# Kernel optimization log

Hardware: AMD Instinct MI355X
Metric: run time of the kernel (lower is better)

Reference implementation:

```python
import jax, jax.numpy as jnp
import numpy as np

N = 100000      # nodes
E = 800000      # edges (avg degree 8)
D_IN = 256      # input feature dim
D_H = 256       # hidden dim (hard-coded in module)
D_OUT = 128     # h_feats


def setup_inputs() -> dict:
    key = jax.random.key(0)
    ks = jax.random.split(key, 8)
    feat = jax.random.normal(ks[0], (N, D_IN), jnp.float32)
    src = jax.random.randint(ks[1], (E,), 0, N, dtype=jnp.int32)
    dst = jax.random.randint(ks[2], (E,), 0, N, dtype=jnp.int32)
    def lin(k, din, dout):
        return jax.random.normal(k, (din, dout), jnp.float32) / np.float32(np.sqrt(din))
    return {
        'feat': feat, 'src': src, 'dst': dst,
        'w_self1': lin(ks[3], D_IN, D_H), 'w_neigh1': lin(ks[4], D_IN, D_H),
        'b1': jnp.zeros((D_H,), jnp.float32),
        'w_self2': lin(ks[5], D_H, D_OUT), 'w_neigh2': lin(ks[6], D_H, D_OUT),
        'b2': jnp.zeros((D_OUT,), jnp.float32),
    }


def _sage_mean(h, src, dst, w_self, w_neigh, b):
    # DGL SAGEConv 'mean': rst = h @ W_self + mean_{in-neighbors}(h) @ W_neigh + b
    ones = jnp.ones((src.shape[0],), h.dtype)
    deg = jax.ops.segment_sum(ones, dst, num_segments=N)          # in-degree per node
    msum = jax.ops.segment_sum(h[src], dst, num_segments=N)      # [N, d] gather-scatter
    mean = msum / jnp.maximum(deg, 1.0)[:, None]                  # zero-degree -> 0
    return h @ w_self + mean @ w_neigh + b


def reference(feat, src, dst, w_self1, w_neigh1, b1, w_self2, w_neigh2, b2):
    h = jax.nn.relu(_sage_mean(feat, src, dst, w_self1, w_neigh1, b1))
    h = jax.nn.relu(_sage_mean(h, src, dst, w_self2, w_neigh2, b2))
    # F.normalize(h, dim=1): x / max(||x||_2, eps)
    norm = jnp.linalg.norm(h, axis=1, keepdims=True)
    return h / jnp.maximum(norm, 1e-12)
```

## Files before the change

### kernel.cpp

```cpp
#include <hip/hip_runtime.h>

#define DIN 256
#define DH  256
#define DOUT 128

typedef __attribute__((ext_vector_type(8))) short bf16x8;
typedef __attribute__((ext_vector_type(4))) float f32x4;
typedef __attribute__((ext_vector_type(2))) float f32x2;
typedef __attribute__((ext_vector_type(4))) unsigned short ushort4v;
typedef __attribute__((ext_vector_type(8))) unsigned short ushort8v;
typedef __attribute__((ext_vector_type(4))) unsigned int uint4v;

static __device__ __forceinline__ unsigned short f2bf(float x) {
    unsigned u = __float_as_uint(x);
    u += 0x7fffu + ((u >> 16) & 1u);
    return (unsigned short)(u >> 16);
}
static __device__ __forceinline__ float bf2f(unsigned short h) {
    return __uint_as_float(((unsigned)h) << 16);
}

static __device__ __forceinline__ void gload16(const unsigned short* g, void* l) {
    __builtin_amdgcn_global_load_lds(
        (const __attribute__((address_space(1))) unsigned int*)g,
        (__attribute__((address_space(3))) unsigned int*)l,
        16, 0, 0);
}

static __device__ __forceinline__ void cvt_unit(const float* __restrict__ feat,
                                                unsigned short* __restrict__ featb,
                                                unsigned int* __restrict__ feat8,
                                                long long i, long long ncHalf) {
    long long i2 = i + ncHalf;
    f32x4 v0 = __builtin_nontemporal_load((const f32x4*)feat + i);
    f32x4 v1 = __builtin_nontemporal_load((const f32x4*)feat + i2);
    ushort4v o0, o1;
    o0[0] = f2bf(v0[0]); o0[1] = f2bf(v0[1]); o0[2] = f2bf(v0[2]); o0[3] = f2bf(v0[3]);
    o1[0] = f2bf(v1[0]); o1[1] = f2bf(v1[1]); o1[2] = f2bf(v1[2]); o1[3] = f2bf(v1[3]);
    *((ushort4v*)featb + i)  = o0;
    *((ushort4v*)featb + i2) = o1;
    int u0 = __builtin_amdgcn_cvt_pk_fp8_f32(v0[0], v0[1], 0, 0);
    u0     = __builtin_amdgcn_cvt_pk_fp8_f32(v0[2], v0[3], u0, 1);
    int u1 = __builtin_amdgcn_cvt_pk_fp8_f32(v1[0], v1[1], 0, 0);
    u1     = __builtin_amdgcn_cvt_pk_fp8_f32(v1[2], v1[3], u1, 1);
    feat8[i]  = (unsigned)u0;
    feat8[i2] = (unsigned)u1;
}

__global__ void countcvt_kernel(const int* __restrict__ dst, int* __restrict__ cnt, int E, int bCnt,
                                const float* __restrict__ feat, unsigned short* __restrict__ featb,
                                unsigned int* __restrict__ feat8, long long ncHalf, int nA) {
    int b = blockIdx.x;
    int t0 = (int)((long long)b * bCnt / nA);
    int t1 = (int)((long long)(b + 1) * bCnt / nA);
    if (t1 > t0) {
        int e = t0 * 256 + threadIdx.x;
        if (e < E) atomicAdd(&cnt[dst[e]], 1);
    } else {
        long long i = (long long)(b - t0) * 256 + threadIdx.x;
        if (i < ncHalf) cvt_unit(feat, featb, feat8, i, ncHalf);
    }
}

__global__ void fillcvt_kernel(const int* __restrict__ src, const int* __restrict__ dst,
                               int* __restrict__ cursor, int* __restrict__ csr, int E, int bFill,
                               const float* __restrict__ feat, unsigned short* __restrict__ featb,
                               unsigned int* __restrict__ feat8, long long ncHalf,
                               int cvtOff, int bCvtB,
                               const float* __restrict__ w_self1, const float* __restrict__ w_neigh1,
                               const float* __restrict__ w_self2, const float* __restrict__ w_neigh2,
                               unsigned short* __restrict__ ws1t, unsigned short* __restrict__ wn1t,
                               unsigned short* __restrict__ wcat, int nB) {
    int b = blockIdx.x;
    int t0 = (int)((long long)b * bFill / nB);
    int t1 = (int)((long long)(b + 1) * bFill / nB);
    if (t1 > t0) {
        int e = t0 * 256 + threadIdx.x;
        if (e < E) {
            int d = dst[e];
            int p = atomicAdd(&cursor[d], 1);
            csr[p] = src[e];
        }
    } else {
        int j = b - t0;
        if (j < bCvtB) {
            long long i = (long long)(cvtOff + j) * 256 + threadIdx.x;
            if (i < ncHalf) cvt_unit(feat, featb, feat8, i, ncHalf);
        } else {
            int idx = (j - bCvtB) * 256 + threadIdx.x;
            if (idx < 65536) {
                int nn = idx >> 8, k = idx & 255;
                ws1t[idx] = f2bf(w_self1[k * 256 + nn]);
            } else if (idx < 131072) {
                int jj = idx - 65536; int nn = jj >> 8, k = jj & 255;
                wn1t[jj] = f2bf(w_neigh1[k * 256 + nn]);
            } else if (idx < 163840) {
                int jj = idx - 131072; int nn = jj >> 8, k = jj & 255;
                wcat[jj] = f2bf(w_neigh2[k * 128 + nn]);
            } else if (idx < 196608) {
                int jj = idx - 163840; int nn = jj >> 8, k = jj & 255;
                wcat[32768 + jj] = f2bf(w_self2[k * 128 + nn]);
            }
        }
    }
}

__global__ void block_sums_kernel(const int* __restrict__ cnt, int* __restrict__ partial, int N) {
    __shared__ int sdata[256];
    int t = threadIdx.x;
    int base = blockIdx.x * 1024;
    int s = 0;
#pragma unroll
    for (int j = 0; j < 4; ++j) {
        int i = base + t * 4 + j;
        if (i < N) s += cnt[i];
    }
    sdata[t] = s; __syncthreads();
    for (int o = 128; o; o >>= 1) {
        if (t < o) sdata[t] += sdata[t + o];
        __syncthreads();
    }
    if (t == 0) partial[blockIdx.x] = sdata[0];
}

__global__ void scan_block_kernel(int* __restrict__ cnt, const int* __restrict__ partial,
                                  int* __restrict__ off, int N, int E, int nb) {
    __shared__ int sdata[256];
    __shared__ int pbase;
    int b = blockIdx.x, t = threadIdx.x;

    int pv = (t < nb) ? partial[t] : 0;
    sdata[t] = pv; __syncthreads();
    for (int o = 1; o < 256; o <<= 1) {
        int y = (t >= o) ? sdata[t - o] : 0;
        __syncthreads();
        sdata[t] += y;
        __syncthreads();
    }
    if (t == 0) pbase = (b == 0) ? 0 : sdata[b - 1];
    __syncthreads();
    int base0 = pbase;
    __syncthreads();

    int base = b * 1024;
    int vals[4]; int local = 0;
#pragma unroll
    for (int j = 0; j < 4; ++j) {
        int i = base + t * 4 + j;
        vals[j] = (i < N) ? cnt[i] : 0;
        local += vals[j];
    }
    sdata[t] = local; __syncthreads();
    for (int o = 1; o < 256; o <<= 1) {
        int y = (t >= o) ? sdata[t - o] : 0;
        __syncthreads();
        sdata[t] += y;
        __syncthreads();
    }
    int run = sdata[t] - local + base0;
#pragma unroll
    for (int j = 0; j < 4; ++j) {
        int i = base + t * 4 + j;
        if (i < N) { off[i] = run; cnt[i] = run; }
        run += vals[j];
    }
    if (b == 0 && t == 0) off[N] = E;
}

__global__ void gather_mean256_kernel(const unsigned int* __restrict__ feat8, const int* __restrict__ off,
                                      const int* __restrict__ csr, unsigned short* __restrict__ agg, int N) {
    int wid  = (int)((blockIdx.x * (long long)blockDim.x + threadIdx.x) >> 6);
    int lane = threadIdx.x & 63;
    if (wid >= N) return;
    int start = off[wid], end = off[wid + 1];
    const int g   = lane >> 4;
    const int cl  = lane & 15;
    float a[16] = {};
    int e = start;
    for (; e + 7 < end; e += 8) {
        int s0 = csr[e + g], s1 = csr[e + 4 + g];
        uint4v v0 = *(const uint4v*)(feat8 + (long long)s0 * 64 + cl * 4);
        uint4v v1 = *(const uint4v*)(feat8 + (long long)s1 * 64 + cl * 4);
#pragma unroll
        for (int d = 0; d < 4; ++d) {
            f32x2 p0 = __builtin_amdgcn_cvt_pk_f32_fp8((int)v0[d], false);
            f32x2 p1 = __builtin_amdgcn_cvt_pk_f32_fp8((int)v0[d], true);
            f32x2 q0 = __builtin_amdgcn_cvt_pk_f32_fp8((int)v1[d], false);
            f32x2 q1 = __builtin_amdgcn_cvt_pk_f32_fp8((int)v1[d], true);
            a[d * 4 + 0] += p0[0] + q0[0];
            a[d * 4 + 1] += p0[1] + q0[1];
            a[d * 4 + 2] += p1[0] + q1[0];
            a[d * 4 + 3] += p1[1] + q1[1];
        }
    }
    for (; e < end; e += 4) {
        int idx = e + g;
        if (idx < end) {
            int s = csr[idx];
            uint4v v = *(const uint4v*)(feat8 + (long long)s * 64 + cl * 4);
#pragma unroll
            for (int d = 0; d < 4; ++d) {
                f32x2 p0 = __builtin_amdgcn_cvt_pk_f32_fp8((int)v[d], false);
                f32x2 p1 = __builtin_amdgcn_cvt_pk_f32_fp8((int)v[d], true);
                a[d * 4 + 0] += p0[0];
                a[d * 4 + 1] += p0[1];
                a[d * 4 + 2] += p1[0];
                a[d * 4 + 3] += p1[1];
            }
        }
    }
#pragma unroll
    for (int j = 0; j < 16; ++j) {
        a[j] += __shfl_xor(a[j], 16);
        a[j] += __shfl_xor(a[j], 32);
    }
    if (g == 0) {
        float inv = 1.0f / (float)max(end - start, 1);
        ushort8v o0, o1;
#pragma unroll
        for (int j = 0; j < 8; ++j) { o0[j] = f2bf(a[j] * inv); o1[j] = f2bf(a[8 + j] * inv); }
        unsigned short* dstp = agg + (long long)wid * 256 + cl * 16;
        *(ushort8v*)dstp       = o0;
        *(ushort8v*)(dstp + 8) = o1;
    }
}

__global__ __launch_bounds__(512)
void gemm1_kernel(const unsigned short* __restrict__ A,  const unsigned short* __restrict__ WT,
                  const unsigned short* __restrict__ A2, const unsigned short* __restrict__ WT2,
                  const float* __restrict__ bias, unsigned short* __restrict__ C, int M)
{
    const int K = 256;
    __shared__ __align__(16) char lds[2][24576];

    const int tid = threadIdx.x;
    const int wid = tid >> 6, lane = tid & 63;
    const int l15 = lane & 15, lg = lane >> 4;
    const int wr = wid >> 2, wc = wid & 3;
    const int row0 = blockIdx.x * 128;

    long long asrc; int adst;
    {
        int c = tid, r = c >> 2, s = c & 3;
        int kc = s ^ ((r >> 1) & 3);
        asrc = (long long)min(row0 + r, M - 1) * K + kc * 8;
        adst = c * 16;
    }
    long long bsrc[2]; int bdst[2];
#pragma unroll
    for (int i = 0; i < 2; ++i) {
        int c = wid * 128 + i * 64 + lane, r = c >> 2, s = c & 3;
        int kc = s ^ ((r >> 1) & 3);
        bsrc[i] = (long long)r * K + kc * 8;
        bdst[i] = 8192 + c * 16;
    }

    const int slot = (lg ^ ((l15 >> 1) & 3)) * 16;
    int aoff[4], boff[4];
#pragma unroll
    for (int m = 0; m < 4; ++m) aoff[m] = (wr * 64 + m * 16 + l15) * 64 + slot;
#pragma unroll
    for (int n = 0; n < 4; ++n) boff[n] = 8192 + (wc * 64 + n * 16 + l15) * 64 + slot;

    f32x4 acc[4][4] = {};

    auto stage = [&](int buf, int t) {
        const unsigned short* Ap = (t >= 8) ? A2 : A;
        const unsigned short* Wp = (t >= 8) ? WT2 : WT;
        int k0 = (t & 7) * 32;
        gload16(Ap + asrc + k0, &lds[buf][adst]);
        gload16(Wp + bsrc[0] + k0, &lds[buf][bdst[0]]);
        gload16(Wp + bsrc[1] + k0, &lds[buf][bdst[1]]);
    };

    stage(0, 0);
    __syncthreads();

    for (int t = 0; t < 16; ++t) {
        const int cur = t & 1;
        if (t + 1 < 16) stage(cur ^ 1, t + 1);
        const char* L = lds[cur];
        bf16x8 af[4], bfr[4];
#pragma unroll
        for (int m = 0; m < 4; ++m) af[m]  = *(const bf16x8*)(L + aoff[m]);
#pragma unroll
        for (int n = 0; n < 4; ++n) bfr[n] = *(const bf16x8*)(L + boff[n]);
#pragma unroll
        for (int m = 0; m < 4; ++m)
#pragma unroll
            for (int n = 0; n < 4; ++n)
                acc[m][n] = __builtin_amdgcn_mfma_f32_16x16x32_bf16(af[m], bfr[n], acc[m][n], 0, 0, 0);
        __syncthreads();
    }

#pragma unroll
    for (int m = 0; m < 4; ++m) {
#pragma unroll
        for (int rr = 0; rr < 4; ++rr) {
            int grow = row0 + wr * 64 + m * 16 + lg * 4 + rr;
            if (grow >= M) continue;
#pragma unroll
            for (int n = 0; n < 4; ++n) {
                int gcol = wc * 64 + n * 16 + l15;
                float v = fmaxf(acc[m][n][rr] + bias[gcol], 0.f);
                C[(long long)grow * 256 + gcol] = f2bf(v);
            }
        }
    }
}

__global__ __launch_bounds__(512)
void gemm23_kernel(const unsigned short* __restrict__ A, const unsigned short* __restrict__ WT,
                   const float* __restrict__ b2,
                   unsigned short* __restrict__ p2, unsigned short* __restrict__ self2, int M)
{
    const int K = 256;
    __shared__ __align__(16) char lds[2][24576];

    const int tid = threadIdx.x;
    const int wid = tid >> 6, lane = tid & 63;
    const int l15 = lane & 15, lg = lane >> 4;
    const int wr = wid >> 2, wc = wid & 3;
    const int row0 = blockIdx.x * 128;

    long long asrc; int adst;
    {
        int c = tid, r = c >> 2, s = c & 3;
        int kc = s ^ ((r >> 1) & 3);
        asrc = (long long)min(row0 + r, M - 1) * K + kc * 8;
        adst = c * 16;
    }
    long long bsrc[2]; int bdst[2];
#pragma unroll
    for (int i = 0; i < 2; ++i) {
        int c = wid * 128 + i * 64 + lane, r = c >> 2, s = c & 3;
        int kc = s ^ ((r >> 1) & 3);
        bsrc[i] = (long long)r * K + kc * 8;
        bdst[i] = 8192 + c * 16;
    }

    const int slot = (lg ^ ((l15 >> 1) & 3)) * 16;
    int aoff[4], boff[4];
#pragma unroll
    for (int m = 0; m < 4; ++m) aoff[m] = (wr * 64 + m * 16 + l15) * 64 + slot;
#pragma unroll
    for (int n = 0; n < 4; ++n) boff[n] = 8192 + (wc * 64 + n * 16 + l15) * 64 + slot;

    f32x4 acc[4][4] = {};

    auto stage = [&](int buf, int t) {
        int k0 = t * 32;
        gload16(A  + asrc + k0, &lds[buf][adst]);
        gload16(WT + bsrc[0] + k0, &lds[buf][bdst[0]]);
        gload16(WT + bsrc[1] + k0, &lds[buf][bdst[1]]);
    };

    stage(0, 0);
    __syncthreads();

    for (int t = 0; t < 8; ++t) {
        const int cur = t & 1;
        if (t + 1 < 8) stage(cur ^ 1, t + 1);
        const char* L = lds[cur];
        bf16x8 af[4], bfr[4];
#pragma unroll
        for (int m = 0; m < 4; ++m) af[m]  = *(const bf16x8*)(L + aoff[m]);
#pragma unroll
        for (int n = 0; n < 4; ++n) bfr[n] = *(const bf16x8*)(L + boff[n]);
#pragma unroll
        for (int m = 0; m < 4; ++m)
#pragma unroll
            for (int n = 0; n < 4; ++n)
                acc[m][n] = __builtin_amdgcn_mfma_f32_16x16x32_bf16(af[m], bfr[n], acc[m][n], 0, 0, 0);
        __syncthreads();
    }

    if (wc < 2) {
#pragma unroll
        for (int m = 0; m < 4; ++m)
#pragma unroll
            for (int rr = 0; rr < 4; ++rr) {
                int grow = row0 + wr * 64 + m * 16 + lg * 4 + rr;
                if (grow >= M) continue;
#pragma unroll
                for (int n = 0; n < 4; ++n) {
                    int col = wc * 64 + n * 16 + l15;
                    p2[(long long)grow * 128 + col] = f2bf(acc[m][n][rr]);
                }
            }
    } else {
        float bv[4];
#pragma unroll
        for (int n = 0; n < 4; ++n) bv[n] = b2[(wc - 2) * 64 + n * 16 + l15];
#pragma unroll
        for (int m = 0; m < 4; ++m)
#pragma unroll
            for (int rr = 0; rr < 4; ++rr) {
                int grow = row0 + wr * 64 + m * 16 + lg * 4 + rr;
                if (grow >= M) continue;
#pragma unroll
                for (int n = 0; n < 4; ++n) {
                    int col = (wc - 2) * 64 + n * 16 + l15;
                    self2[(long long)grow * 128 + col] = f2bf(acc[m][n][rr] + bv[n]);
                }
            }
    }
}

__global__ void gather_final_kernel(const unsigned short* __restrict__ p2, const int* __restrict__ off,
                                    const int* __restrict__ csr, const unsigned short* __restrict__ self2,
                                    float* __restrict__ out, int N) {
    int wid  = (int)((blockIdx.x * (long long)blockDim.x + threadIdx.x) >> 6);
    int lane = threadIdx.x & 63;
    if (wid >= N) return;
    int start = off[wid], end = off[wid + 1];
    const int g  = lane >> 4;
    const int c8 = (lane & 15) * 8;
    float a[8] = {};
    int e = start;
    for (; e + 7 < end; e += 8) {
        int s0 = csr[e + g], s1 = csr[e + 4 + g];
        ushort8v v0 = *(const ushort8v*)(p2 + (long long)s0 * 128 + c8);
        ushort8v v1 = *(const ushort8v*)(p2 + (long long)s1 * 128 + c8);
#pragma unroll
        for (int j = 0; j < 8; ++j) a[j] += bf2f(v0[j]) + bf2f(v1[j]);
    }
    for (; e < end; e += 4) {
        int idx = e + g;
        if (idx < end) {
            int s = csr[idx];
            ushort8v v = *(const ushort8v*)(p2 + (long long)s * 128 + c8);
#pragma unroll
            for (int j = 0; j < 8; ++j) a[j] += bf2f(v[j]);
        }
    }
#pragma unroll
    for (int j = 0; j < 8; ++j) {
        a[j] += __shfl_xor(a[j], 16);
        a[j] += __shfl_xor(a[j], 32);
    }
    float invd = 1.0f / (float)max(end - start, 1);
    ushort8v sv = *(const ushort8v*)(self2 + (long long)wid * 128 + c8);
    float v[8];
    float ss = 0.f;
#pragma unroll
    for (int j = 0; j < 8; ++j) {
        v[j] = fmaxf(bf2f(sv[j]) + a[j] * invd, 0.f);
        ss += v[j] * v[j];
    }
    ss += __shfl_xor(ss, 1);
    ss += __shfl_xor(ss, 2);
    ss += __shfl_xor(ss, 4);
    ss += __shfl_xor(ss, 8);
    float inv = 1.0f / fmaxf(sqrtf(ss), 1e-12f);
    if (g == 0) {
        f32x4 o0 = { v[0] * inv, v[1] * inv, v[2] * inv, v[3] * inv };
        f32x4 o1 = { v[4] * inv, v[5] * inv, v[6] * inv, v[7] * inv };
        float* dstp = out + (long long)wid * 128 + c8;
        __builtin_nontemporal_store(o0, (f32x4*)dstp);
        __builtin_nontemporal_store(o1, (f32x4*)(dstp + 4));
    }
}

extern "C" void kernel_launch(void* const* d_in, const int* in_sizes, int n_in,
                              void* d_out, int out_size, void* d_ws, size_t ws_size,
                              hipStream_t stream) {
    const float* feat     = (const float*)d_in[0];
    const int*   src      = (const int*)  d_in[1];
    const int*   dst      = (const int*)  d_in[2];
    const float* w_self1  = (const float*)d_in[3];
    const float* w_neigh1 = (const float*)d_in[4];
    const float* b1       = (const float*)d_in[5];
    const float* w_self2  = (const float*)d_in[6];
    const float* w_neigh2 = (const float*)d_in[7];
    const float* b2       = (const float*)d_in[8];
    float* out = (float*)d_out;

    const int N = in_sizes[0] / DIN;
    const int E = in_sizes[1];

    char* ws = (char*)d_ws;
    auto a4k = [](size_t x) { return (x + 4095) & ~(size_t)4095; };
    size_t o = 0;
    int* cnt  = (int*)(ws + o); o += a4k((size_t)N * 4);
    int* off  = (int*)(ws + o); o += a4k((size_t)(N + 1) * 4);
    int* part = (int*)(ws + o); o += a4k(1024);
    int* csr  = (int*)(ws + o); o += a4k((size_t)E * 4);
    unsigned short* ws1t = (unsigned short*)(ws + o); o += a4k((size_t)DIN * DH * 2);
    unsigned short* wn1t = (unsigned short*)(ws + o); o += a4k((size_t)DIN * DH * 2);
    unsigned short* wcat = (unsigned short*)(ws + o); o += a4k((size_t)256 * 256 * 2);
    unsigned int*   feat8 = (unsigned int*)(ws + o); o += a4k((size_t)N * DIN);
    unsigned short* featb = (unsigned short*)(ws + o); o += a4k((size_t)N * DIN * 2);
    unsigned short* aggb  = (unsigned short*)(ws + o); o += a4k((size_t)N * DIN * 2);
    unsigned short* h1b   = (unsigned short*)(ws + o); o += a4k((size_t)N * DH * 2);

    unsigned short* p2b    = featb;
    unsigned short* self2b = aggb;

    const int nblk = (N + 1023) / 1024;

    long long ncHalf = (long long)N * DIN / 8;
    const int bCvtTot = (int)((ncHalf + 255) / 256);
    const int bCvtA = 7000;
    const int bCvtB = bCvtTot - bCvtA;
    const int bAtom = (E + 255) / 256;
    const int bWt   = 768;

    hipMemsetAsync(cnt, 0, (size_t)N * 4, stream);
    const int nA = bCvtA + bAtom;
    countcvt_kernel<<<nA, 256, 0, stream>>>(dst, cnt, E, bAtom, feat, featb, feat8, ncHalf, nA);

    block_sums_kernel<<<nblk, 256, 0, stream>>>(cnt, part, N);
    scan_block_kernel<<<nblk, 256, 0, stream>>>(cnt, part, off, N, E, nblk);

    const int nB = bCvtB + bWt + bAtom;
    fillcvt_kernel<<<nB, 256, 0, stream>>>(
        src, dst, cnt, csr, E, bAtom,
        feat, featb, feat8, ncHalf, bCvtA, bCvtB,
        w_self1, w_neigh1, w_self2, w_neigh2, ws1t, wn1t, wcat, nB);

    const int mblk = (N + 127) / 128;

    gather_mean256_kernel<<<(N + 3) / 4, 256, 0, stream>>>(feat8, off, csr, aggb, N);
    gemm1_kernel<<<mblk, 512, 0, stream>>>(featb, ws1t, aggb, wn1t, b1, h1b, N);

    gemm23_kernel<<<mblk, 512, 0, stream>>>(h1b, wcat, b2, p2b, self2b, N);
    gather_final_kernel<<<(N + 3) / 4, 256, 0, stream>>>(p2b, off, csr, self2b, out, N);
}
```

Measured before the change: 256.3 us.

## Replace two-pass prefix scan with single-pass decoupled lookback scan

Merges the block-sums and block-scan kernels into one kernel that uses decoupled lookback: each block publishes its aggregate and inclusive prefix through status flags. This removes one kernel launch and a redundant re-read of the counts. The status flags sit right after the count array and are zeroed by the same memset. The conversion-work split between the count and fill kernels is also rebalanced. The lookback relies on blocks being scheduled in order, which holds in practice because there are only about 98 blocks.

```diff
diff --git a/kernel.cpp b/kernel.cpp
--- a/kernel.cpp
+++ b/kernel.cpp
@@ -60,6 +60,59 @@
         long long i = (long long)(b - t0) * 256 + threadIdx.x;
         if (i < ncHalf) cvt_unit(feat, featb, feat8, i, ncHalf);
     }
+}
+
+__global__ void scan_lookback_kernel(int* __restrict__ cnt, int* __restrict__ status,
+                                     int* __restrict__ aggbuf, int* __restrict__ inclbuf,
+                                     int* __restrict__ off, int N, int E, int nb) {
+    __shared__ int sdata[256];
+    __shared__ int sbase;
+    int b = blockIdx.x, t = threadIdx.x;
+    int base = b * 1024;
+    int vals[4]; int local = 0;
+#pragma unroll
+    for (int j = 0; j < 4; ++j) {
+        int i = base + t * 4 + j;
+        vals[j] = (i < N) ? cnt[i] : 0;
+        local += vals[j];
+    }
+    sdata[t] = local; __syncthreads();
+    for (int o = 1; o < 256; o <<= 1) {
+        int y = (t >= o) ? sdata[t - o] : 0;
+        __syncthreads();
+        sdata[t] += y;
+        __syncthreads();
+    }
+    int total = sdata[255];
+
+    if (t == 0) {
+        aggbuf[b] = total;
+        __threadfence();
+        atomicExch(&status[b], 1);
+        int acc = 0;
+        for (int j = b - 1; j >= 0; --j) {
+            int s;
+            while ((s = atomicAdd(&status[j], 0)) == 0) { }
+            __threadfence();
+            if (s == 2) { acc += inclbuf[j]; break; }
+            acc += aggbuf[j];
+        }
+        inclbuf[b] = acc + total;
+        __threadfence();
+        atomicExch(&status[b], 2);
+        sbase = acc;
+    }
+    __syncthreads();
+    int base0 = sbase;
+
+    int run = sdata[t] - local + base0;
+#pragma unroll
+    for (int j = 0; j < 4; ++j) {
+        int i = base + t * 4 + j;
+        if (i < N) { off[i] = run; cnt[i] = run; }
+        run += vals[j];
+    }
+    if (b == 0 && t == 0) off[N] = E;
 }
 
 __global__ void fillcvt_kernel(const int* __restrict__ src, const int* __restrict__ dst,
@@ -105,68 +158,6 @@
     }
 }
 
-__global__ void block_sums_kernel(const int* __restrict__ cnt, int* __restrict__ partial, int N) {
-    __shared__ int sdata[256];
-    int t = threadIdx.x;
-    int base = blockIdx.x * 1024;
-    int s = 0;
-#pragma unroll
-    for (int j = 0; j < 4; ++j) {
-        int i = base + t * 4 + j;
-        if (i < N) s += cnt[i];
-    }
-    sdata[t] = s; __syncthreads();
-    for (int o = 128; o; o >>= 1) {
-        if (t < o) sdata[t] += sdata[t + o];
-        __syncthreads();
-    }
-    if (t == 0) partial[blockIdx.x] = sdata[0];
-}
-
-__global__ void scan_block_kernel(int* __restrict__ cnt, const int* __restrict__ partial,
-                                  int* __restrict__ off, int N, int E, int nb) {
-    __shared__ int sdata[256];
-    __shared__ int pbase;
-    int b = blockIdx.x, t = threadIdx.x;
-
-    int pv = (t < nb) ? partial[t] : 0;
-    sdata[t] = pv; __syncthreads();
-    for (int o = 1; o < 256; o <<= 1) {
-        int y = (t >= o) ? sdata[t - o] : 0;
-        __syncthreads();
-        sdata[t] += y;
-        __syncthreads();
-    }
-    if (t == 0) pbase = (b == 0) ? 0 : sdata[b - 1];
-    __syncthreads();
-    int base0 = pbase;
-    __syncthreads();
-
-    int base = b * 1024;
-    int vals[4]; int local = 0;
-#pragma unroll
-    for (int j = 0; j < 4; ++j) {
-        int i = base + t * 4 + j;
-        vals[j] = (i < N) ? cnt[i] : 0;
-        local += vals[j];
-    }
-    sdata[t] = local; __syncthreads();
-    for (int o = 1; o < 256; o <<= 1) {
-        int y = (t >= o) ? sdata[t - o] : 0;
-        __syncthreads();
-        sdata[t] += y;
-        __syncthreads();
-    }
-    int run = sdata[t] - local + base0;
-#pragma unroll
-    for (int j = 0; j < 4; ++j) {
-        int i = base + t * 4 + j;
-        if (i < N) { off[i] = run; cnt[i] = run; }
-        run += vals[j];
-    }
-    if (b == 0 && t == 0) off[N] = E;
-}
-
 __global__ void gather_mean256_kernel(const unsigned int* __restrict__ feat8, const int* __restrict__ off,
                                       const int* __restrict__ csr, unsigned short* __restrict__ agg, int N) {
     int wid  = (int)((blockIdx.x * (long long)blockDim.x + threadIdx.x) >> 6);
@@ -482,7 +473,8 @@
     char* ws = (char*)d_ws;
     auto a4k = [](size_t x) { return (x + 4095) & ~(size_t)4095; };
     size_t o = 0;
-    int* cnt  = (int*)(ws + o); o += a4k((size_t)N * 4);
+    int* cnt    = (int*)(ws + o); o += (size_t)N * 4;
+    int* status = (int*)(ws + o); o = a4k(o + 128 * 4);
     int* off  = (int*)(ws + o); o += a4k((size_t)(N + 1) * 4);
     int* part = (int*)(ws + o); o += a4k(1024);
     int* csr  = (int*)(ws + o); o += a4k((size_t)E * 4);
@@ -494,6 +486,9 @@
     unsigned short* aggb  = (unsigned short*)(ws + o); o += a4k((size_t)N * DIN * 2);
     unsigned short* h1b   = (unsigned short*)(ws + o); o += a4k((size_t)N * DH * 2);
 
+    int* aggbuf  = part;
+    int* inclbuf = part + 128;
+
     unsigned short* p2b    = featb;
     unsigned short* self2b = aggb;
 
@@ -501,17 +496,16 @@
 
     long long ncHalf = (long long)N * DIN / 8;
     const int bCvtTot = (int)((ncHalf + 255) / 256);
-    const int bCvtA = 7000;
+    const int bCvtA = 5500;
     const int bCvtB = bCvtTot - bCvtA;
     const int bAtom = (E + 255) / 256;
     const int bWt   = 768;
 
-    hipMemsetAsync(cnt, 0, (size_t)N * 4, stream);
+    hipMemsetAsync(cnt, 0, ((size_t)N + 128) * 4, stream);
     const int nA = bCvtA + bAtom;
     countcvt_kernel<<<nA, 256, 0, stream>>>(dst, cnt, E, bAtom, feat, featb, feat8, ncHalf, nA);
 
-    block_sums_kernel<<<nblk, 256, 0, stream>>>(cnt, part, N);
-    scan_block_kernel<<<nblk, 256, 0, stream>>>(cnt, part, off, N, E, nblk);
+    scan_lookback_kernel<<<nblk, 256, 0, stream>>>(cnt, status, aggbuf, inclbuf, off, N, E, nblk);
 
     const int nB = bCvtB + bWt + bAtom;
     fillcvt_kernel<<<nB, 256, 0, stream>>>(
```

Result: slower. 283.3 us (+10.5%).
